# Kernel optimization log

Measured on AMD Instinct MI355X. Metric: run time of the kernel, lower is better.

Reference implementation:

```python
import jax, jax.numpy as jnp
import numpy as np

NDIGIT = 10
DIM_IN = 256
DIM_OUT = 784
BATCH = 16384


def setup_inputs() -> dict:
    key = jax.random.key(0)
    k_theta, k_label, k_W = jax.random.split(key, 3)
    theta = jax.random.normal(k_theta, (BATCH, DIM_IN), dtype=jnp.float32)
    label = jax.random.randint(k_label, (BATCH,), 0, NDIGIT, dtype=jnp.int32)
    # xavier_uniform for each (dim_out, dim_in) matrix
    limit = float(np.sqrt(6.0 / (DIM_IN + DIM_OUT)))
    megaW = jax.random.uniform(k_W, (NDIGIT, DIM_OUT, DIM_IN), dtype=jnp.float32,
                               minval=-limit, maxval=limit)
    megab = jnp.zeros((NDIGIT, DIM_OUT), dtype=jnp.float32)
    return {"theta": theta, "label": label, "megaW": megaW, "megab": megab}


def reference(theta, label, megaW, megab):
    # Dense compute across all 10 digit experts (matches torch.bmm over repeated theta)
    # added: [b, ndigit, dim_out]
    added = jnp.einsum('ndi,bi->bnd', megaW, theta) + megab[None, :, :]
    # Select the expert output per example by label (vector_gather)
    selected = jnp.take_along_axis(added, label[:, None, None].astype(jnp.int32), axis=1)[:, 0, :]
    probs = jax.nn.sigmoid(selected)
    return probs
```

## Files before the change

kernel.cpp:

```cpp
#include <hip/hip_runtime.h>
#include <hip/hip_bf16.h>

#define NDIGIT 10
#define DIM_IN 256
#define DIM_OUT 784
#define BATCH 16384
#define BM 64
#define BN 112
#define NCB 7
#define MAX_MT (BATCH / BM + NDIGIT)
#define G9_BLOCKS (MAX_MT * NCB)
#define QB 14336

#define WS_IDX 1024
#define WS_DESC 600
#define WS_WBF_BYTES 69632
#define WS_TH_BYTES (WS_WBF_BYTES + 2007040 * 2)

typedef __attribute__((ext_vector_type(4))) float f32x4;
typedef __attribute__((ext_vector_type(8))) short bf16x8;

__device__ __forceinline__ short f2bf(float f) {
    union { float f; unsigned u; } c; c.f = f;
    unsigned u = c.u;
    u += 0x7fffu + ((u >> 16) & 1u);
    return (short)(u >> 16);
}

__device__ __forceinline__ void gload16(const void* gp, void* lp) {
    __builtin_amdgcn_global_load_lds(
        (const __attribute__((address_space(1))) void*)gp,
        (__attribute__((address_space(3))) void*)lp, 16, 0, 0);
}

__global__ void prep_k(const float* __restrict__ megaW,
                       const int* __restrict__ label,
                       int* __restrict__ wsi,
                       short* __restrict__ wbf) {
    int b = blockIdx.x, t = threadIdx.x;
    if (b < 980) {
        int base = b * 2048 + t * 8;
        f32x4 v0 = *(const f32x4*)(megaW + base);
        f32x4 v1 = *(const f32x4*)(megaW + base + 4);
        bf16x8 o;
        o[0] = f2bf(v0[0]); o[1] = f2bf(v0[1]); o[2] = f2bf(v0[2]); o[3] = f2bf(v0[3]);
        o[4] = f2bf(v1[0]); o[5] = f2bf(v1[1]); o[6] = f2bf(v1[2]); o[7] = f2bf(v1[3]);
        *(bf16x8*)(wbf + base) = o;
    } else {
        __shared__ int h[NDIGIT];
        int j = b - 980;
        if (t < NDIGIT) h[t] = 0;
        __syncthreads();
        int i0 = j * 512;
        atomicAdd(&h[label[i0 + t]], 1);
        atomicAdd(&h[label[i0 + 256 + t]], 1);
        __syncthreads();
        if (t < NDIGIT) wsi[64 + j * 16 + t] = h[t];
    }
}

__global__ void scatter2_k(const int* __restrict__ label, int* __restrict__ wsi) {
    __shared__ int tot[NDIGIT], bef[NDIGIT], base[NDIGIT + 1], cur[NDIGIT], toff[NDIGIT + 1];
    int j = blockIdx.x, t = threadIdx.x;
    if (t < NDIGIT) {
        int s = 0, sb = 0;
        for (int jj = 0; jj < 32; ++jj) {
            int v = wsi[64 + jj * 16 + t];
            s += v;
            if (jj < j) sb += v;
        }
        tot[t] = s; bef[t] = sb;
    }
    __syncthreads();
    if (t == 0) {
        int off = 0, tf = 0;
        for (int g = 0; g < NDIGIT; ++g) {
            base[g] = off; toff[g] = tf;
            off += tot[g]; tf += (tot[g] + BM - 1) / BM;
        }
        base[NDIGIT] = off; toff[NDIGIT] = tf;
    }
    __syncthreads();
    if (t < NDIGIT) cur[t] = base[t] + bef[t];
    if (j == 0) {
        int ptotal = toff[NDIGIT];
        for (int p = t; p < ptotal; p += 512) {
            int g2 = 0;
            while (p >= toff[g2 + 1]) ++g2;
            int row0 = (p - toff[g2]) * BM;
            int rcv = tot[g2] - row0; if (rcv > BM) rcv = BM;
            wsi[WS_DESC + p] = (base[g2] + row0) | (rcv << 14) | (g2 << 21);
        }
        if (t == 0) wsi[24] = ptotal;
    }
    __syncthreads();
    int i = j * 512 + t;
    int g = label[i];
    int r = atomicAdd(&cur[g], 1);
    wsi[WS_IDX + r] = i;
    if (j == 0 && t < NDIGIT) wsi[t] = base[t];
    if (j == 0 && t == 0) wsi[10] = base[NDIGIT];
}

__global__ void gth_k(const float* __restrict__ theta,
                      const int* __restrict__ wsi,
                      short* __restrict__ thsort) {
    int gid = blockIdx.x * 256 + threadIdx.x;
    int r = gid >> 5;
    int c8 = (gid & 31) << 3;
    int src = wsi[WS_IDX + r];
    const float* p = theta + (size_t)src * DIM_IN + c8;
    f32x4 v0 = *(const f32x4*)p;
    f32x4 v1 = *(const f32x4*)(p + 4);
    bf16x8 o;
    o[0] = f2bf(v0[0]); o[1] = f2bf(v0[1]); o[2] = f2bf(v0[2]); o[3] = f2bf(v0[3]);
    o[4] = f2bf(v1[0]); o[5] = f2bf(v1[1]); o[6] = f2bf(v1[2]); o[7] = f2bf(v1[3]);
    *(bf16x8*)(thsort + (size_t)r * DIM_IN + c8) = o;
}

__device__ __forceinline__ void stage_q(const char* Wcb, int q, char* Bq, int tid) {
#pragma unroll
    for (int it = 0; it < 4; ++it) {
        int chunk = it * 256 + tid;
        if (chunk >= 896) chunk -= 128;
        int lbyte = chunk << 4;
        int L = lbyte ^ ((((lbyte >> 7) & 7)) << 4);
        int row = L >> 7, koff = L & 127;
        gload16(Wcb + row * 512 + q * 128 + koff, Bq + lbyte);
    }
}

#define COMPUTE(Q) do {                                                        \
    _Pragma("unroll")                                                          \
    for (int ksl = 0; ksl < 2; ++ksl) {                                        \
        _Pragma("unroll")                                                      \
        for (int ns = 0; ns < NCB; ++ns) {                                     \
            int n_ = ns * 16 + r16;                                            \
            int byte_ = (n_ << 7) + (ksl << 6) + (kg << 4);                    \
            byte_ ^= (n_ & 7) << 4;                                            \
            bf16x8 bfr_ = *(const bf16x8*)(Bs + byte_);                        \
            acc[ns] = __builtin_amdgcn_mfma_f32_16x16x32_bf16(                 \
                a[(Q) * 2 + ksl], bfr_, acc[ns], 0, 0, 0);                     \
        }                                                                      \
    }                                                                          \
} while (0)

__launch_bounds__(256, 8)
__global__ void moe_gemm9_k(const short* __restrict__ thsort,
                            const float* __restrict__ megab,
                            const int* __restrict__ wsi,
                            const short* __restrict__ wbf,
                            float* __restrict__ out) {
    __shared__ char Bs[QB];

    int Bid = blockIdx.x;
    const int q8 = G9_BLOCKS / 8, r8 = G9_BLOCKS % 8;
    int xcd = Bid & 7, slot = Bid >> 3;
    int w = (xcd < r8 ? xcd * (q8 + 1) : r8 * (q8 + 1) + (xcd - r8) * q8) + slot;
    int mt = w / NCB, cb = w % NCB;

    int total = wsi[24];
    if (mt >= total) return;

    int d = wsi[WS_DESC + mt];
    int startRow = d & 0x3FFF;
    int rc = (d >> 14) & 0x7F;
    int g  = d >> 21;

    int tid = threadIdx.x;
    int wv = tid >> 6, l = tid & 63, r16 = l & 15, kg = l >> 4;

    int mloc = wv * 16 + r16; if (mloc >= rc) mloc = rc - 1;
    const short* Ar = thsort + (size_t)(startRow + mloc) * DIM_IN + kg * 8;
    bf16x8 a[8];
#pragma unroll
    for (int ks = 0; ks < 8; ++ks)
        a[ks] = *(const bf16x8*)(Ar + ks * 32);

    const char* Wcb = (const char*)(wbf + ((size_t)g * DIM_OUT + (size_t)cb * BN) * DIM_IN);

    f32x4 acc[NCB];
#pragma unroll
    for (int ns = 0; ns < NCB; ++ns) acc[ns] = (f32x4){0.f, 0.f, 0.f, 0.f};

#pragma unroll
    for (int q = 0; q < 4; ++q) {
        stage_q(Wcb, q, Bs, tid);
        __syncthreads();
        COMPUTE(q);
        if (q < 3) __syncthreads();
    }

    const float* bg = megab + (size_t)g * DIM_OUT + (size_t)cb * BN;
    const int* idxl = wsi + WS_IDX + startRow;
    int rbase = wv * 16 + kg * 4;
    int orow[4];
#pragma unroll
    for (int j = 0; j < 4; ++j)
        orow[j] = (rbase + j < rc) ? idxl[rbase + j] : -1;

#pragma unroll
    for (int ns = 0; ns < NCB; ++ns) {
        int nloc = ns * 16 + r16;
        float bias = bg[nloc];
#pragma unroll
        for (int j = 0; j < 4; ++j) {
            if (orow[j] >= 0) {
                float x = acc[ns][j] + bias;
                out[(size_t)orow[j] * DIM_OUT + cb * BN + nloc] = 1.0f / (1.0f + __expf(-x));
            }
        }
    }
}

extern "C" void kernel_launch(void* const* d_in, const int* in_sizes, int n_in,
                              void* d_out, int out_size, void* d_ws, size_t ws_size,
                              hipStream_t stream) {
    const float* theta = (const float*)d_in[0];
    const int*   label = (const int*)d_in[1];
    const float* megaW = (const float*)d_in[2];
    const float* megab = (const float*)d_in[3];
    float* out = (float*)d_out;
    int* wsi = (int*)d_ws;
    short* wbf    = (short*)((char*)d_ws + WS_WBF_BYTES);
    short* thsort = (short*)((char*)d_ws + WS_TH_BYTES);

    prep_k    <<<1012, 256, 0, stream>>>(megaW, label, wsi, wbf);
    scatter2_k<<<32, 512, 0, stream>>>(label, wsi);
    gth_k     <<<2048, 256, 0, stream>>>(theta, wsi, thsort);
    moe_gemm9_k<<<G9_BLOCKS, 256, 0, stream>>>(thsort, megab, wsi, wbf, out);
}
```

Measured before the change: 52.63 us.

## Pre-swizzle W into MFMA fragment layout and stage full output rows in LDS

The prep kernel now writes bf16 weights in per-lane MFMA B-fragment order, so the GEMM loads B directly into registers with coalesced 16-byte loads instead of staging through LDS. Each block now handles a 16-row tile and loops over all 49 column tiles across its 4 waves, double-buffering the B registers, instead of a 64x112 tile per block. Sigmoid outputs are gathered into an LDS row buffer and written as contiguous f32x4 full rows to the scattered output rows, which improves store coalescing. The trade-off is that each block rereads the whole expert weight slice, so L2 traffic for W rises, and the large LDS row buffer lowers occupancy.

```diff
diff --git a/kernel.cpp b/kernel.cpp
--- a/kernel.cpp
+++ b/kernel.cpp
@@ -5,16 +5,14 @@
 #define DIM_IN 256
 #define DIM_OUT 784
 #define BATCH 16384
-#define BM 64
-#define BN 112
-#define NCB 7
-#define MAX_MT (BATCH / BM + NDIGIT)
-#define G9_BLOCKS (MAX_MT * NCB)
-#define QB 14336
+#define NCT 49
+#define TM 16
+#define MAX_T16 (BATCH / TM + NDIGIT)
+#define RBS 788
 
 #define WS_IDX 1024
-#define WS_DESC 600
-#define WS_WBF_BYTES 69632
+#define WS_DESC 17408
+#define WS_WBF_BYTES 81920
 #define WS_TH_BYTES (WS_WBF_BYTES + 2007040 * 2)
 
 typedef __attribute__((ext_vector_type(4))) float f32x4;
@@ -25,12 +23,6 @@
     unsigned u = c.u;
     u += 0x7fffu + ((u >> 16) & 1u);
     return (short)(u >> 16);
-}
-
-__device__ __forceinline__ void gload16(const void* gp, void* lp) {
-    __builtin_amdgcn_global_load_lds(
-        (const __attribute__((address_space(1))) void*)gp,
-        (__attribute__((address_space(3))) void*)lp, 16, 0, 0);
 }
 
 __global__ void prep_k(const float* __restrict__ megaW,
@@ -39,13 +31,21 @@
                        short* __restrict__ wbf) {
     int b = blockIdx.x, t = threadIdx.x;
     if (b < 980) {
-        int base = b * 2048 + t * 8;
-        f32x4 v0 = *(const f32x4*)(megaW + base);
-        f32x4 v1 = *(const f32x4*)(megaW + base + 4);
+        int idx = b * 256 + t;
+        int gi = idx >> 9;
+        int ks = (idx >> 6) & 7;
+        int l  = idx & 63;
+        int g  = gi / 49;
+        int ct = gi - g * 49;
+        int col = ct * 16 + (l & 15);
+        int k   = ks * 32 + ((l >> 4) << 3);
+        const float* src = megaW + ((size_t)(g * DIM_OUT + col) * DIM_IN + k);
+        f32x4 v0 = *(const f32x4*)src;
+        f32x4 v1 = *(const f32x4*)(src + 4);
         bf16x8 o;
         o[0] = f2bf(v0[0]); o[1] = f2bf(v0[1]); o[2] = f2bf(v0[2]); o[3] = f2bf(v0[3]);
         o[4] = f2bf(v1[0]); o[5] = f2bf(v1[1]); o[6] = f2bf(v1[2]); o[7] = f2bf(v1[3]);
-        *(bf16x8*)(wbf + base) = o;
+        *(bf16x8*)(wbf + (size_t)idx * 8) = o;
     } else {
         __shared__ int h[NDIGIT];
         int j = b - 980;
@@ -76,7 +76,7 @@
         int off = 0, tf = 0;
         for (int g = 0; g < NDIGIT; ++g) {
             base[g] = off; toff[g] = tf;
-            off += tot[g]; tf += (tot[g] + BM - 1) / BM;
+            off += tot[g]; tf += (tot[g] + TM - 1) / TM;
         }
         base[NDIGIT] = off; toff[NDIGIT] = tf;
     }
@@ -87,19 +87,18 @@
         for (int p = t; p < ptotal; p += 512) {
             int g2 = 0;
             while (p >= toff[g2 + 1]) ++g2;
-            int row0 = (p - toff[g2]) * BM;
-            int rcv = tot[g2] - row0; if (rcv > BM) rcv = BM;
+            int row0 = (p - toff[g2]) * TM;
+            int rcv = tot[g2] - row0; if (rcv > TM) rcv = TM;
             wsi[WS_DESC + p] = (base[g2] + row0) | (rcv << 14) | (g2 << 21);
         }
-        if (t == 0) wsi[24] = ptotal;
+        if (t < NDIGIT) wsi[t] = base[t];
+        if (t == 0) { wsi[10] = base[NDIGIT]; wsi[24] = ptotal; }
     }
     __syncthreads();
     int i = j * 512 + t;
     int g = label[i];
     int r = atomicAdd(&cur[g], 1);
     wsi[WS_IDX + r] = i;
-    if (j == 0 && t < NDIGIT) wsi[t] = base[t];
-    if (j == 0 && t == 0) wsi[10] = base[NDIGIT];
 }
 
 __global__ void gth_k(const float* __restrict__ theta,
@@ -118,51 +117,44 @@
     *(bf16x8*)(thsort + (size_t)r * DIM_IN + c8) = o;
 }
 
-__device__ __forceinline__ void stage_q(const char* Wcb, int q, char* Bq, int tid) {
-#pragma unroll
-    for (int it = 0; it < 4; ++it) {
-        int chunk = it * 256 + tid;
-        if (chunk >= 896) chunk -= 128;
-        int lbyte = chunk << 4;
-        int L = lbyte ^ ((((lbyte >> 7) & 7)) << 4);
-        int row = L >> 7, koff = L & 127;
-        gload16(Wcb + row * 512 + q * 128 + koff, Bq + lbyte);
-    }
-}
-
-#define COMPUTE(Q) do {                                                        \
+
+#define LOADB(B, CT) do {                                                      \
+    const short* Bt_ = Wg + (size_t)(CT) * 4096 + l * 8;                       \
     _Pragma("unroll")                                                          \
-    for (int ksl = 0; ksl < 2; ++ksl) {                                        \
-        _Pragma("unroll")                                                      \
-        for (int ns = 0; ns < NCB; ++ns) {                                     \
-            int n_ = ns * 16 + r16;                                            \
-            int byte_ = (n_ << 7) + (ksl << 6) + (kg << 4);                    \
-            byte_ ^= (n_ & 7) << 4;                                            \
-            bf16x8 bfr_ = *(const bf16x8*)(Bs + byte_);                        \
-            acc[ns] = __builtin_amdgcn_mfma_f32_16x16x32_bf16(                 \
-                a[(Q) * 2 + ksl], bfr_, acc[ns], 0, 0, 0);                     \
-        }                                                                      \
+    for (int ks = 0; ks < 8; ++ks)                                             \
+        (B)[ks] = *(const bf16x8*)(Bt_ + ks * 512);                            \
+} while (0)
+
+#define TILE13(B, CT) do {                                                     \
+    float bias_ = bgb[(CT) * 16 + r16];                                        \
+    f32x4 acc_ = {0.f, 0.f, 0.f, 0.f};                                         \
+    _Pragma("unroll")                                                          \
+    for (int ks = 0; ks < 8; ++ks)                                             \
+        acc_ = __builtin_amdgcn_mfma_f32_16x16x32_bf16(a[ks], (B)[ks], acc_, 0, 0, 0); \
+    _Pragma("unroll")                                                          \
+    for (int j = 0; j < 4; ++j) {                                              \
+        float x_ = acc_[j] + bias_;                                            \
+        rowbuf[(kg * 4 + j) * RBS + (CT) * 16 + r16] = 1.0f / (1.0f + __expf(-x_)); \
     }                                                                          \
 } while (0)
 
-__launch_bounds__(256, 8)
-__global__ void moe_gemm9_k(const short* __restrict__ thsort,
-                            const float* __restrict__ megab,
-                            const int* __restrict__ wsi,
-                            const short* __restrict__ wbf,
-                            float* __restrict__ out) {
-    __shared__ char Bs[QB];
+__launch_bounds__(256, 3)
+__global__ void moe_gemm13_k(const short* __restrict__ thsort,
+                             const float* __restrict__ megab,
+                             const int* __restrict__ wsi,
+                             const short* __restrict__ wbf,
+                             float* __restrict__ out) {
+    __shared__ float rowbuf[TM * RBS];
 
     int Bid = blockIdx.x;
-    const int q8 = G9_BLOCKS / 8, r8 = G9_BLOCKS % 8;
+    const int q8 = MAX_T16 / 8, r8 = MAX_T16 % 8;
     int xcd = Bid & 7, slot = Bid >> 3;
-    int w = (xcd < r8 ? xcd * (q8 + 1) : r8 * (q8 + 1) + (xcd - r8) * q8) + slot;
-    int mt = w / NCB, cb = w % NCB;
+    int p = (xcd < r8 ? xcd * (q8 + 1) : r8 * (q8 + 1) + (xcd - r8) * q8) + slot;
 
     int total = wsi[24];
-    if (mt >= total) return;
-
-    int d = wsi[WS_DESC + mt];
+    if (p >= total) return;
+
+    int d = wsi[WS_DESC + p];
     int startRow = d & 0x3FFF;
     int rc = (d >> 14) & 0x7F;
     int g  = d >> 21;
@@ -170,44 +162,41 @@
     int tid = threadIdx.x;
     int wv = tid >> 6, l = tid & 63, r16 = l & 15, kg = l >> 4;
 
-    int mloc = wv * 16 + r16; if (mloc >= rc) mloc = rc - 1;
+    int mloc = r16; if (mloc >= rc) mloc = rc - 1;
     const short* Ar = thsort + (size_t)(startRow + mloc) * DIM_IN + kg * 8;
     bf16x8 a[8];
 #pragma unroll
     for (int ks = 0; ks < 8; ++ks)
         a[ks] = *(const bf16x8*)(Ar + ks * 32);
 
-    const char* Wcb = (const char*)(wbf + ((size_t)g * DIM_OUT + (size_t)cb * BN) * DIM_IN);
-
-    f32x4 acc[NCB];
+    const short* Wg  = wbf + (size_t)g * (NCT * 4096);
+    const float* bgb = megab + (size_t)g * DIM_OUT;
+
+    bf16x8 bA[8], bB[8];
+    int ct = wv;
+    LOADB(bA, ct);
+    while (true) {
+        int c1 = ct + 4;
+        if (c1 < NCT) { LOADB(bB, c1); TILE13(bA, ct); }
+        else          { TILE13(bA, ct); break; }
+        int c2 = c1 + 4;
+        if (c2 < NCT) { LOADB(bA, c2); TILE13(bB, c1); }
+        else          { TILE13(bB, c1); break; }
+        ct = c2;
+    }
+
+    __syncthreads();
+
+    const int* idxl = wsi + WS_IDX + startRow;
 #pragma unroll
-    for (int ns = 0; ns < NCB; ++ns) acc[ns] = (f32x4){0.f, 0.f, 0.f, 0.f};
-
-#pragma unroll
-    for (int q = 0; q < 4; ++q) {
-        stage_q(Wcb, q, Bs, tid);
-        __syncthreads();
-        COMPUTE(q);
-        if (q < 3) __syncthreads();
-    }
-
-    const float* bg = megab + (size_t)g * DIM_OUT + (size_t)cb * BN;
-    const int* idxl = wsi + WS_IDX + startRow;
-    int rbase = wv * 16 + kg * 4;
-    int orow[4];
-#pragma unroll
-    for (int j = 0; j < 4; ++j)
-        orow[j] = (rbase + j < rc) ? idxl[rbase + j] : -1;
-
-#pragma unroll
-    for (int ns = 0; ns < NCB; ++ns) {
-        int nloc = ns * 16 + r16;
-        float bias = bg[nloc];
-#pragma unroll
-        for (int j = 0; j < 4; ++j) {
-            if (orow[j] >= 0) {
-                float x = acc[ns][j] + bias;
-                out[(size_t)orow[j] * DIM_OUT + cb * BN + nloc] = 1.0f / (1.0f + __expf(-x));
+    for (int s = 0; s < 13; ++s) {
+        int c = s * 256 + tid;
+        if (c < TM * 196) {
+            int row = c / 196;
+            int cir = c - row * 196;
+            if (row < rc) {
+                f32x4 v = *(const f32x4*)(rowbuf + row * RBS + cir * 4);
+                *(f32x4*)(out + (size_t)idxl[row] * DIM_OUT + cir * 4) = v;
             }
         }
     }
@@ -225,8 +214,8 @@
     short* wbf    = (short*)((char*)d_ws + WS_WBF_BYTES);
     short* thsort = (short*)((char*)d_ws + WS_TH_BYTES);
 
-    prep_k    <<<1012, 256, 0, stream>>>(megaW, label, wsi, wbf);
-    scatter2_k<<<32, 512, 0, stream>>>(label, wsi);
-    gth_k     <<<2048, 256, 0, stream>>>(theta, wsi, thsort);
-    moe_gemm9_k<<<G9_BLOCKS, 256, 0, stream>>>(thsort, megab, wsi, wbf, out);
-}
+    prep_k     <<<1012, 256, 0, stream>>>(megaW, label, wsi, wbf);
+    scatter2_k <<<32, 512, 0, stream>>>(label, wsi);
+    gth_k      <<<2048, 256, 0, stream>>>(theta, wsi, thsort);
+    moe_gemm13_k<<<MAX_T16, 256, 0, stream>>>(thsort, megab, wsi, wbf, out);
+}
```

Result: faster. 49.80 us (-5.4%).

## Double GEMM row tile and stage output through LDS for coalesced stores

Applied to the files above, without the earlier changes.

Raises the row tile from 64 to 128, so each wave computes two 16-row MFMA tiles that share every B fragment read from LDS, halving weight staging per output row. The first weight quarter is now staged before the A-fragment loads so the two overlap. The epilogue writes sigmoid results as bf16 into a per-wave LDS buffer, then reads them back as rows and emits 16-byte float4 stores, replacing scattered 4-byte stores. In exchange, the outputs are rounded to bf16 precision, register pressure is higher, the launch-bounds occupancy hint drops from 8 to 3, and there are fewer blocks.

```diff
diff --git a/kernel.cpp b/kernel.cpp
--- a/kernel.cpp
+++ b/kernel.cpp
@@ -5,12 +5,14 @@
 #define DIM_IN 256
 #define DIM_OUT 784
 #define BATCH 16384
-#define BM 64
+#define BM 128
 #define BN 112
 #define NCB 7
 #define MAX_MT (BATCH / BM + NDIGIT)
-#define G9_BLOCKS (MAX_MT * NCB)
+#define G_BLOCKS (MAX_MT * NCB)
 #define QB 14336
+#define RBSS2 116
+#define LDS_BYTES 14848
 
 #define WS_IDX 1024
 #define WS_DESC 600
@@ -19,6 +21,7 @@
 
 typedef __attribute__((ext_vector_type(4))) float f32x4;
 typedef __attribute__((ext_vector_type(8))) short bf16x8;
+typedef __attribute__((ext_vector_type(4))) unsigned short u16x4;
 
 __device__ __forceinline__ short f2bf(float f) {
     union { float f; unsigned u; } c; c.f = f;
@@ -89,17 +92,16 @@
             while (p >= toff[g2 + 1]) ++g2;
             int row0 = (p - toff[g2]) * BM;
             int rcv = tot[g2] - row0; if (rcv > BM) rcv = BM;
-            wsi[WS_DESC + p] = (base[g2] + row0) | (rcv << 14) | (g2 << 21);
+            wsi[WS_DESC + p] = (base[g2] + row0) | (rcv << 14) | (g2 << 22);
         }
-        if (t == 0) wsi[24] = ptotal;
+        if (t < NDIGIT) wsi[t] = base[t];
+        if (t == 0) { wsi[10] = base[NDIGIT]; wsi[24] = ptotal; }
     }
     __syncthreads();
     int i = j * 512 + t;
     int g = label[i];
     int r = atomicAdd(&cur[g], 1);
     wsi[WS_IDX + r] = i;
-    if (j == 0 && t < NDIGIT) wsi[t] = base[t];
-    if (j == 0 && t == 0) wsi[10] = base[NDIGIT];
 }
 
 __global__ void gth_k(const float* __restrict__ theta,
@@ -130,7 +132,7 @@
     }
 }
 
-#define COMPUTE(Q) do {                                                        \
+#define COMPUTE_Q(Q) do {                                                      \
     _Pragma("unroll")                                                          \
     for (int ksl = 0; ksl < 2; ++ksl) {                                        \
         _Pragma("unroll")                                                      \
@@ -139,22 +141,56 @@
             int byte_ = (n_ << 7) + (ksl << 6) + (kg << 4);                    \
             byte_ ^= (n_ & 7) << 4;                                            \
             bf16x8 bfr_ = *(const bf16x8*)(Bs + byte_);                        \
-            acc[ns] = __builtin_amdgcn_mfma_f32_16x16x32_bf16(                 \
-                a[(Q) * 2 + ksl], bfr_, acc[ns], 0, 0, 0);                     \
+            acc0[ns] = __builtin_amdgcn_mfma_f32_16x16x32_bf16(                \
+                a0[(Q) * 2 + ksl], bfr_, acc0[ns], 0, 0, 0);                   \
+            acc1[ns] = __builtin_amdgcn_mfma_f32_16x16x32_bf16(                \
+                a1[(Q) * 2 + ksl], bfr_, acc1[ns], 0, 0, 0);                   \
         }                                                                      \
     }                                                                          \
 } while (0)
 
-__launch_bounds__(256, 8)
-__global__ void moe_gemm9_k(const short* __restrict__ thsort,
-                            const float* __restrict__ megab,
-                            const int* __restrict__ wsi,
-                            const short* __restrict__ wbf,
-                            float* __restrict__ out) {
-    __shared__ char Bs[QB];
+#define EPI_PASS(P, ACC) do {                                                  \
+    _Pragma("unroll")                                                          \
+    for (int ns = 0; ns < NCB; ++ns) {                                         \
+        int col_ = ns * 16 + r16;                                              \
+        float bias_ = bg[col_];                                                \
+        _Pragma("unroll")                                                      \
+        for (int j = 0; j < 4; ++j) {                                          \
+            float x_ = (ACC)[ns][j] + bias_;                                   \
+            rb[(kg * 4 + j) * RBSS2 + col_] = f2bf(1.0f / (1.0f + __expf(-x_))); \
+        }                                                                      \
+    }                                                                          \
+    asm volatile("s_waitcnt lgkmcnt(0)" ::: "memory");                         \
+    __builtin_amdgcn_sched_barrier(0);                                         \
+    {                                                                          \
+        const int* idxl_ = wsi + WS_IDX + startRow + wv * 32 + (P) * 16;       \
+        _Pragma("unroll")                                                      \
+        for (int it = 0; it < 7; ++it) {                                       \
+            int c_ = it * 64 + l;               \
+            int row_ = c_ / 28;                                                \
+            int cir_ = c_ - row_ * 28;                                         \
+            if (wv * 32 + (P) * 16 + row_ < rc) {                              \
+                u16x4 v_ = *(const u16x4*)(rb + row_ * RBSS2 + cir_ * 4);      \
+                union { unsigned u; float f; } e0, e1, e2, e3;                 \
+                e0.u = (unsigned)v_[0] << 16; e1.u = (unsigned)v_[1] << 16;    \
+                e2.u = (unsigned)v_[2] << 16; e3.u = (unsigned)v_[3] << 16;    \
+                f32x4 o_ = { e0.f, e1.f, e2.f, e3.f };                         \
+                *(f32x4*)(out + (size_t)idxl_[row_] * DIM_OUT + cb * BN + cir_ * 4) = o_; \
+            }                                                                  \
+        }                                                                      \
+    }                                                                          \
+} while (0)
+
+__launch_bounds__(256, 3)
+__global__ void moe_gemm15_k(const short* __restrict__ thsort,
+                             const float* __restrict__ megab,
+                             const int* __restrict__ wsi,
+                             const short* __restrict__ wbf,
+                             float* __restrict__ out) {
+    __shared__ char Bs[LDS_BYTES];
 
     int Bid = blockIdx.x;
-    const int q8 = G9_BLOCKS / 8, r8 = G9_BLOCKS % 8;
+    const int q8 = G_BLOCKS / 8, r8 = G_BLOCKS % 8;
     int xcd = Bid & 7, slot = Bid >> 3;
     int w = (xcd < r8 ? xcd * (q8 + 1) : r8 * (q8 + 1) + (xcd - r8) * q8) + slot;
     int mt = w / NCB, cb = w % NCB;
@@ -164,53 +200,56 @@
 
     int d = wsi[WS_DESC + mt];
     int startRow = d & 0x3FFF;
-    int rc = (d >> 14) & 0x7F;
-    int g  = d >> 21;
+    int rc = (d >> 14) & 0xFF;
+    int g  = d >> 22;
 
     int tid = threadIdx.x;
     int wv = tid >> 6, l = tid & 63, r16 = l & 15, kg = l >> 4;
 
-    int mloc = wv * 16 + r16; if (mloc >= rc) mloc = rc - 1;
-    const short* Ar = thsort + (size_t)(startRow + mloc) * DIM_IN + kg * 8;
-    bf16x8 a[8];
+    const char* Wcb = (const char*)(wbf + ((size_t)g * DIM_OUT + (size_t)cb * BN) * DIM_IN);
+
+    stage_q(Wcb, 0, Bs, tid);
+
+    int m0 = wv * 32 + r16;      if (m0 >= rc) m0 = rc - 1;
+    int m1 = wv * 32 + 16 + r16; if (m1 >= rc) m1 = rc - 1;
+    const short* Ar0 = thsort + (size_t)(startRow + m0) * DIM_IN + kg * 8;
+    const short* Ar1 = thsort + (size_t)(startRow + m1) * DIM_IN + kg * 8;
+    bf16x8 a0[8], a1[8];
 #pragma unroll
-    for (int ks = 0; ks < 8; ++ks)
-        a[ks] = *(const bf16x8*)(Ar + ks * 32);
-
-    const char* Wcb = (const char*)(wbf + ((size_t)g * DIM_OUT + (size_t)cb * BN) * DIM_IN);
-
-    f32x4 acc[NCB];
-#pragma unroll
-    for (int ns = 0; ns < NCB; ++ns) acc[ns] = (f32x4){0.f, 0.f, 0.f, 0.f};
-
-#pragma unroll
-    for (int q = 0; q < 4; ++q) {
-        stage_q(Wcb, q, Bs, tid);
-        __syncthreads();
-        COMPUTE(q);
-        if (q < 3) __syncthreads();
-    }
-
-    const float* bg = megab + (size_t)g * DIM_OUT + (size_t)cb * BN;
-    const int* idxl = wsi + WS_IDX + startRow;
-    int rbase = wv * 16 + kg * 4;
-    int orow[4];
-#pragma unroll
-    for (int j = 0; j < 4; ++j)
-        orow[j] = (rbase + j < rc) ? idxl[rbase + j] : -1;
-
+    for (int ks = 0; ks < 8; ++ks) {
+        a0[ks] = *(const bf16x8*)(Ar0 + ks * 32);
+        a1[ks] = *(const bf16x8*)(Ar1 + ks * 32);
+    }
+
+    f32x4 acc0[NCB], acc1[NCB];
 #pragma unroll
     for (int ns = 0; ns < NCB; ++ns) {
-        int nloc = ns * 16 + r16;
-        float bias = bg[nloc];
-#pragma unroll
-        for (int j = 0; j < 4; ++j) {
-            if (orow[j] >= 0) {
-                float x = acc[ns][j] + bias;
-                out[(size_t)orow[j] * DIM_OUT + cb * BN + nloc] = 1.0f / (1.0f + __expf(-x));
-            }
-        }
-    }
+        acc0[ns] = (f32x4){0.f, 0.f, 0.f, 0.f};
+        acc1[ns] = (f32x4){0.f, 0.f, 0.f, 0.f};
+    }
+
+    __syncthreads();
+    COMPUTE_Q(0);
+    __syncthreads();
+    stage_q(Wcb, 1, Bs, tid);
+    __syncthreads();
+    COMPUTE_Q(1);
+    __syncthreads();
+    stage_q(Wcb, 2, Bs, tid);
+    __syncthreads();
+    COMPUTE_Q(2);
+    __syncthreads();
+    stage_q(Wcb, 3, Bs, tid);
+    __syncthreads();
+    COMPUTE_Q(3);
+    __syncthreads();
+
+    const float* bg = megab + (size_t)g * DIM_OUT + (size_t)cb * BN;
+    short* rb = (short*)Bs + wv * (16 * RBSS2);
+    EPI_PASS(0, acc0);
+    asm volatile("s_waitcnt lgkmcnt(0)" ::: "memory");
+    __builtin_amdgcn_sched_barrier(0);
+    EPI_PASS(1, acc1);
 }
 
 extern "C" void kernel_launch(void* const* d_in, const int* in_sizes, int n_in,
@@ -225,8 +264,8 @@
     short* wbf    = (short*)((char*)d_ws + WS_WBF_BYTES);
     short* thsort = (short*)((char*)d_ws + WS_TH_BYTES);
 
-    prep_k    <<<1012, 256, 0, stream>>>(megaW, label, wsi, wbf);
-    scatter2_k<<<32, 512, 0, stream>>>(label, wsi);
-    gth_k     <<<2048, 256, 0, stream>>>(theta, wsi, thsort);
-    moe_gemm9_k<<<G9_BLOCKS, 256, 0, stream>>>(thsort, megab, wsi, wbf, out);
-}
+    prep_k      <<<1012, 256, 0, stream>>>(megaW, label, wsi, wbf);
+    scatter2_k  <<<32, 512, 0, stream>>>(label, wsi);
+    gth_k       <<<2048, 256, 0, stream>>>(theta, wsi, thsort);
+    moe_gemm15_k<<<G_BLOCKS, 256, 0, stream>>>(thsort, megab, wsi, wbf, out);
+}
```

Result: faster. 46.81 us (-11.1%).
